# Optimization experiments

Hardware: AMD Instinct MI355X
Metric: run time of the kernel (lower is better)

## Reference

```python
import jax, jax.numpy as jnp
import numpy as np

B, T, D, H, CL = 2, 4096, 2048, 16, 512
DK = D // H          # key_dim == head_dim (value_factor=1) == 128
SCALING = DK ** -0.5


def _rel_pos():
    # RetNet relative position: per-head decay gamma, rotary sin/cos, chunk decay masks
    h = np.arange(H, dtype=np.float64)
    gamma = 1.0 - 2.0 ** (-5.0 - h)                           # (H,)
    angle = 1.0 / (10000.0 ** (np.arange(0, DK, 2) / DK))
    angle = np.repeat(angle, 2)                               # (DK,) each freq duplicated
    pos = np.arange(T)[:, None] * angle[None, :]              # (T, DK)
    sin, cos = np.sin(pos), np.cos(pos)
    idx = np.arange(CL)
    expn = idx[:, None] - idx[None, :]                        # (CL, CL)
    m = np.where(expn >= 0, gamma[:, None, None] ** np.maximum(expn, 0), 0.0)  # (H,CL,CL)
    scale = np.sqrt(m.sum(-1, keepdims=True))                 # (H,CL,1)
    mask = m / scale
    cross_decay = (gamma ** CL)[:, None, None]                # (H,1,1)
    inner = gamma[:, None] ** (idx + 1)                       # (H,CL)
    inner_decay = inner[:, :, None] / (scale / mask[:, -1].sum(-1)[:, None, None])  # (H,CL,1)
    f32 = lambda a: jnp.asarray(a, jnp.float32)
    return f32(sin), f32(cos), f32(mask), f32(cross_decay), f32(inner_decay)


def setup_inputs() -> dict:
    key = jax.random.key(0)
    kx, kq, kk, kv, kg, ko = jax.random.split(key, 6)
    sin, cos, mask, cross_decay, inner_decay = _rel_pos()
    mk = lambda k: jax.random.normal(k, (D, D), jnp.float32) * 0.02  # ~xavier w/ small gain
    z = jnp.zeros((D,), jnp.float32)
    return dict(
        x=jax.random.normal(kx, (B, T, D), jnp.float32),
        sin=sin, cos=cos, mask=mask, cross_decay=cross_decay, inner_decay=inner_decay,
        wq=mk(kq), bq=z, wk=mk(kk), bk=z, wv=mk(kv), bv=z, wg=mk(kg), bg=z,
        wo=jax.random.normal(ko, (D, D), jnp.float32) * (1.0 / np.sqrt(D)), bo=z,
    )


def _rotate_every_two(x):
    x1, x2 = x[..., ::2], x[..., 1::2]
    return jnp.stack((-x2, x1), axis=-1).reshape(x.shape)


def _theta_shift(x, sin, cos):
    return x * cos + _rotate_every_two(x) * sin


def reference(x, sin, cos, mask, cross_decay, inner_decay,
              wq, bq, wk, bk, wv, bv, wg, bg, wo, bo):
    NC = T // CL
    q = (x @ wq.T + bq).reshape(B, T, H, DK).transpose(0, 2, 1, 3)           # (B,H,T,DK)
    k = ((x @ wk.T + bk) * SCALING).reshape(B, T, H, DK).transpose(0, 2, 1, 3)
    v = x @ wv.T + bv                                                        # (B,T,D)
    g = x @ wg.T + bg
    qr = _theta_shift(q, sin, cos)
    kr = _theta_shift(k, sin, cos)
    # chunk views -> (B, NC, H, CL, DK)
    qr = qr.reshape(B, H, NC, CL, DK).transpose(0, 2, 1, 3, 4)
    kr = kr.reshape(B, H, NC, CL, DK).transpose(0, 2, 1, 3, 4)
    vc = v.reshape(B, NC, CL, H, DK).transpose(0, 1, 3, 2, 4)                # (B,NC,H,CL,HD)
    # intra-chunk decay-masked attention
    qk = jnp.einsum('bnhld,bnhmd->bnhlm', qr, kr) * mask                      # (B,NC,H,CL,CL)
    inner_scale = jnp.clip(jnp.abs(jax.lax.stop_gradient(qk)).sum(-1, keepdims=True), 1.0)
    inner_out = jnp.einsum('bnhlm,bnhmd->bnhld', qk / inner_scale, vc)
    # per-chunk KV contribution (keys weighted by remaining decay = last mask row)
    kv = jnp.einsum('bnhlk,bnhld->bnhkd', kr, vc * mask[:, -1, :, None])      # (B,NC,H,DK,HD)

    def step(carry, kv_i):
        kv_state, kv_scale = carry
        out = (kv_state / kv_scale, kv_scale)
        new_state = kv_state * cross_decay + kv_i
        s = jnp.abs(jax.lax.stop_gradient(new_state)).sum(-2, keepdims=True)
        new_scale = jnp.clip(s.max(-1, keepdims=True), 1.0)
        return (new_state, new_scale), out

    init = (jnp.zeros((B, H, DK, DK), x.dtype), jnp.ones((B, H, 1, 1), x.dtype))
    _, (kv_rec, cross_scale) = jax.lax.scan(step, init, jnp.moveaxis(kv, 1, 0))
    kv_rec = jnp.moveaxis(kv_rec, 0, 1)            # (B,NC,H,DK,HD)
    cross_scale = jnp.moveaxis(cross_scale, 0, 1)  # (B,NC,H,1,1)
    all_scale = jnp.maximum(inner_scale, cross_scale)
    cross_out = jnp.einsum('bnhlk,bnhkd->bnhld', qr * inner_decay, kv_rec)
    out = inner_out / (all_scale / inner_scale) + cross_out / (all_scale / cross_scale)
    out = out.transpose(0, 1, 3, 2, 4)             # (B,NC,CL,H,HD)
    # group_norm: LayerNorm over head_dim, no affine, eps=1e-6
    mu = out.mean(-1, keepdims=True)
    var = ((out - mu) ** 2).mean(-1, keepdims=True)
    out = (out - mu) / jnp.sqrt(var + 1e-6)
    out = out.reshape(B, T, D)
    out = jax.nn.silu(g) * out                     # swish gate
    return out @ wo.T + bo
```

## Files before the change

### kernel.cpp

```cpp
#include <hip/hip_runtime.h>
#include <hip/hip_bf16.h>
#include <math.h>

#define NB   2
#define NT   4096
#define ND   2048
#define NH   16
#define NDK  128
#define NCL  512
#define NNC  8
#define NTOK 8192
#define SCALING 0.08838834764831845f

typedef unsigned short u16;
typedef short short8 __attribute__((ext_vector_type(8)));
typedef unsigned short ushort8 __attribute__((ext_vector_type(8)));
typedef float f32x4 __attribute__((ext_vector_type(4)));
typedef float float4v __attribute__((ext_vector_type(4)));
typedef short short4v __attribute__((ext_vector_type(4)));

__device__ __forceinline__ float bf2f(u16 u) {
    union { unsigned int i; float f; } v; v.i = ((unsigned int)u) << 16; return v.f;
}
__device__ __forceinline__ u16 f2bf(float f) {
    union { float f; unsigned int i; } v; v.f = f;
    unsigned int r = v.i + 0x7FFFu + ((v.i >> 16) & 1u);
    return (u16)(r >> 16);
}

__device__ __forceinline__ void gload16(const void* g, void* l) {
    __builtin_amdgcn_global_load_lds(
        (const __attribute__((address_space(1))) unsigned int*)g,
        (__attribute__((address_space(3))) unsigned int*)l, 16, 0, 0);
}

#define MFMA16(acc_, a_, b_) acc_ = __builtin_amdgcn_mfma_f32_16x16x32_bf16(a_, b_, acc_, 0, 0, 0)

__device__ __forceinline__ void gemm_bt_core(
    const u16* __restrict__ A, const u16* __restrict__ Bm,
    int lda, int ldb, int K, u16* As, u16* Bs, f32x4 acc[4][4])
{
    const int tid  = threadIdx.x;
    const int lane = tid & 63;
    const int lr   = lane & 15;
    const int lg   = lane >> 4;
    const int wid  = tid >> 6;
    const int wr   = (wid >> 1) * 64;
    const int wc   = (wid & 1) * 64;
    const int swz  = lr & 7;
    const int uc0  = ((0 * 4 + lg) ^ swz) * 8;
    const int uc1  = ((1 * 4 + lg) ^ swz) * 8;

    for (int kt = 0; kt < K; kt += 64) {
#pragma unroll
        for (int i = 0; i < 4; ++i) {
            int c = tid + i * 256;
            int row = c >> 3, u = c & 7;
            int col = (u ^ (row & 7)) * 8;
            gload16(A  + (size_t)row * lda + kt + col, As + (size_t)c * 8);
            gload16(Bm + (size_t)row * ldb + kt + col, Bs + (size_t)c * 8);
        }
        __syncthreads();
#pragma unroll
        for (int kk = 0; kk < 2; ++kk) {
            const int uc = kk ? uc1 : uc0;
            short8 a[4], b[4];
#pragma unroll
            for (int m = 0; m < 4; ++m)
                a[m] = *(const short8*)(As + (size_t)(wr + m * 16 + lr) * 64 + uc);
#pragma unroll
            for (int n = 0; n < 4; ++n)
                b[n] = *(const short8*)(Bs + (size_t)(wc + n * 16 + lr) * 64 + uc);
#pragma unroll
            for (int m = 0; m < 4; ++m)
#pragma unroll
                for (int n = 0; n < 4; ++n)
                    MFMA16(acc[m][n], a[m], b[n]);
        }
        __syncthreads();
    }
}

__global__ __launch_bounds__(256) void k_f2bf(const float* __restrict__ src,
                                              u16* __restrict__ dst, int n4)
{
    int i = blockIdx.x * blockDim.x + threadIdx.x;
    int stride = gridDim.x * blockDim.x;
    for (int j = i; j < n4; j += stride) {
        float4v f = *(const float4v*)(src + (size_t)j * 4);
        short4v o;
        o.x = (short)f2bf(f.x); o.y = (short)f2bf(f.y);
        o.z = (short)f2bf(f.z); o.w = (short)f2bf(f.w);
        *(short4v*)(dst + (size_t)j * 4) = o;
    }
}

__global__ __launch_bounds__(256) void k_gemm1(
    const u16* __restrict__ xb, const u16* __restrict__ wb,
    const float* __restrict__ bq, const float* __restrict__ bk,
    const float* __restrict__ bv, const float* __restrict__ bg,
    const float* __restrict__ sinp, const float* __restrict__ cosp,
    const float* __restrict__ maskp,
    u16* __restrict__ qro, u16* __restrict__ kro, u16* __restrict__ krwT,
    u16* __restrict__ vT, u16* __restrict__ glin)
{
    __shared__ __align__(16) u16 As[128 * 64];
    __shared__ __align__(16) u16 Bs[128 * 64];
    f32x4 acc[4][4];
#pragma unroll
    for (int m = 0; m < 4; ++m)
#pragma unroll
        for (int n = 0; n < 4; ++n) acc[m][n] = (f32x4){0.f, 0.f, 0.f, 0.f};

    int bid = blockIdx.x;
    int swzb = (bid & 7) * 512 + (bid >> 3);
    int mt = swzb >> 6, nt = swzb & 63;

    gemm_bt_core(xb + (size_t)mt * 128 * ND, wb + (size_t)nt * 128 * ND,
                 ND, ND, ND, As, Bs, acc);

    int tid = threadIdx.x, lane = tid & 63, lr = lane & 15, lg = lane >> 4, wid = tid >> 6;
    int wr = (wid >> 1) * 64, wc = (wid & 1) * 64;
    int which = nt >> 4;

    if (which <= 1) {
        const float* bias = (which == 0) ? bq : bk;
#pragma unroll
        for (int m = 0; m < 4; ++m) {
#pragma unroll
            for (int n = 0; n < 4; ++n) {
#pragma unroll
                for (int r = 0; r < 4; ++r) {
                    int row = mt * 128 + wr + m * 16 + lg * 4 + r;
                    int col = nt * 128 + wc + n * 16 + lr;
                    int f = col & 2047, h = f >> 7, d = f & 127;
                    int b = row >> 12, t = row & 4095, cn = t >> 9, cl = t & 511;
                    float v = acc[m][n][r] + bias[f];
                    if (which == 1) v *= SCALING;
                    float sv = sinp[(size_t)t * NDK + d];
                    float cv = cosp[(size_t)t * NDK + d];
                    float vp = __shfl_xor(v, 1);
                    float rot = (lr & 1) ? vp : -vp;
                    float o = v * cv + rot * sv;
                    size_t chbase = (size_t)(b * NNC + cn) * NH + h;
                    if (which == 0) {
                        qro[(chbase * NCL + cl) * NDK + d] = f2bf(o);
                    } else {
                        kro[(chbase * NCL + cl) * NDK + d] = f2bf(o);
                        float w = maskp[((size_t)h * NCL + (NCL - 1)) * NCL + cl];
                        krwT[(chbase * NDK + d) * NCL + cl] = f2bf(o * w);
                    }
                }
            }
        }
    } else {
#pragma unroll
        for (int m = 0; m < 4; ++m) {
#pragma unroll
            for (int n = 0; n < 4; ++n) {
#pragma unroll
                for (int r = 0; r < 4; ++r) {
                    int row = mt * 128 + wr + m * 16 + lg * 4 + r;
                    int col = nt * 128 + wc + n * 16 + lr;
                    int f = col & 2047;
                    float v = acc[m][n][r];
                    if (which == 2) {
                        int h = f >> 7, d = f & 127;
                        int b = row >> 12, t = row & 4095, cn = t >> 9, cl = t & 511;
                        vT[(((size_t)(b * NNC + cn) * NH + h) * NDK + d) * NCL + cl] = f2bf(v + bv[f]);
                    } else {
                        glin[(size_t)row * ND + f] = f2bf(v + bg[f]);
                    }
                }
            }
        }
    }
}

__global__ __launch_bounds__(256) void k_gemm2(
    const u16* __restrict__ y, const u16* __restrict__ wob,
    const float* __restrict__ bo, float* __restrict__ out)
{
    __shared__ __align__(16) u16 As[128 * 64];
    __shared__ __align__(16) u16 Bs[128 * 64];
    f32x4 acc[4][4];
#pragma unroll
    for (int m = 0; m < 4; ++m)
#pragma unroll
        for (int n = 0; n < 4; ++n) acc[m][n] = (f32x4){0.f, 0.f, 0.f, 0.f};

    int bid = blockIdx.x;
    int swzb = (bid & 7) * 128 + (bid >> 3);
    int mt = swzb >> 4, nt = swzb & 15;

    gemm_bt_core(y + (size_t)mt * 128 * ND, wob + (size_t)nt * 128 * ND,
                 ND, ND, ND, As, Bs, acc);

    int tid = threadIdx.x, lane = tid & 63, lr = lane & 15, lg = lane >> 4, wid = tid >> 6;
    int wr = (wid >> 1) * 64, wc = (wid & 1) * 64;
#pragma unroll
    for (int m = 0; m < 4; ++m)
#pragma unroll
        for (int n = 0; n < 4; ++n)
#pragma unroll
            for (int r = 0; r < 4; ++r) {
                int row = mt * 128 + wr + m * 16 + lg * 4 + r;
                int col = nt * 128 + wc + n * 16 + lr;
                out[(size_t)row * ND + col] = acc[m][n][r] + bo[col];
            }
}

__global__ __launch_bounds__(256) void k_inner(
    const u16* __restrict__ qr, const u16* __restrict__ kr,
    const u16* __restrict__ vT, const float* __restrict__ mask,
    float* __restrict__ iraw, float* __restrict__ iscale)
{
    __shared__ __align__(16) u16 Qs[128 * 128];
    __shared__ __align__(16) u16 Ks[32 * 128];
    __shared__ __align__(16) u16 Vs[128 * 32];
    __shared__ __align__(16) u16 Ps[4][32 * 32];
    __shared__ float sl[128];

    int qt = blockIdx.x, bnh = blockIdx.y;
    int h = bnh & 15;
    const u16* Q = qr + (size_t)bnh * NCL * NDK + (size_t)qt * 128 * NDK;
    const u16* K = kr + (size_t)bnh * NCL * NDK;
    const u16* V = vT + (size_t)bnh * NDK * NCL;
    const float* M = mask + (size_t)h * NCL * NCL + (size_t)qt * 128 * NCL;

    int tid = threadIdx.x, lane = tid & 63, lr = lane & 15, lg = lane >> 4, wid = tid >> 6;
    if (tid < 128) sl[tid] = 0.f;
#pragma unroll
    for (int i = 0; i < 8; ++i) {
        int c = tid + i * 256;
        gload16(Q + (size_t)c * 8, (char*)Qs + (size_t)c * 16);
    }
    __syncthreads();

    short8 aq[2][4];
#pragma unroll
    for (int i = 0; i < 2; ++i)
#pragma unroll
        for (int kk = 0; kk < 4; ++kk)
            aq[i][kk] = *(const short8*)(Qs + (wid * 32 + i * 16 + lr) * 128 + kk * 32 + lg * 8);

    f32x4 acc[2][8];
#pragma unroll
    for (int i = 0; i < 2; ++i)
#pragma unroll
        for (int n = 0; n < 8; ++n) acc[i][n] = (f32x4){0.f, 0.f, 0.f, 0.f};

    int msteps = qt * 4 + 4;
    for (int ms = 0; ms < msteps; ++ms) {
        int mb = ms * 32;
#pragma unroll
        for (int i = 0; i < 2; ++i) {
            int c = tid + i * 256;
            int row = c >> 4, cc = (c & 15) * 8;
            gload16(K + (size_t)(mb + row) * NDK + cc, (char*)Ks + (size_t)c * 16);
        }
#pragma unroll
        for (int i = 0; i < 2; ++i) {
            int c = tid + i * 256;
            int row = c >> 2, cc = (c & 3) * 8;
            gload16(V + (size_t)row * NCL + mb + cc, (char*)Vs + (size_t)c * 16);
        }
        __syncthreads();

        f32x4 pa[2][2];
#pragma unroll
        for (int i = 0; i < 2; ++i) { pa[i][0] = (f32x4){0.f,0.f,0.f,0.f}; pa[i][1] = (f32x4){0.f,0.f,0.f,0.f}; }
#pragma unroll
        for (int kk = 0; kk < 4; ++kk) {
            short8 bk0 = *(const short8*)(Ks + (lr) * 128 + kk * 32 + lg * 8);
            short8 bk1 = *(const short8*)(Ks + (16 + lr) * 128 + kk * 32 + lg * 8);
#pragma unroll
            for (int i = 0; i < 2; ++i) {
                pa[i][0] = __builtin_amdgcn_mfma_f32_16x16x32_bf16(aq[i][kk], bk0, pa[i][0], 0, 0, 0);
                pa[i][1] = __builtin_amdgcn_mfma_f32_16x16x32_bf16(aq[i][kk], bk1, pa[i][1], 0, 0, 0);
            }
        }
#pragma unroll
        for (int i = 0; i < 2; ++i) {
#pragma unroll
            for (int r = 0; r < 4; ++r) {
                int rloc = i * 16 + lg * 4 + r;
                int row128 = wid * 32 + rloc;
                float m0 = M[(size_t)row128 * NCL + mb + lr];
                float m1 = M[(size_t)row128 * NCL + mb + 16 + lr];
                float p0 = pa[i][0][r] * m0;
                float p1 = pa[i][1][r] * m1;
                float ss = fabsf(p0) + fabsf(p1);
                ss += __shfl_xor(ss, 1); ss += __shfl_xor(ss, 2);
                ss += __shfl_xor(ss, 4); ss += __shfl_xor(ss, 8);
                if (lr == 0) sl[row128] += ss;
                Ps[wid][rloc * 32 + lr]      = f2bf(p0);
                Ps[wid][rloc * 32 + 16 + lr] = f2bf(p1);
            }
        }
        __syncthreads();

        short8 ap[2];
#pragma unroll
        for (int i = 0; i < 2; ++i)
            ap[i] = *(const short8*)(Ps[wid] + (i * 16 + lr) * 32 + lg * 8);
#pragma unroll
        for (int n = 0; n < 8; ++n) {
            short8 bv8 = *(const short8*)(Vs + (n * 16 + lr) * 32 + lg * 8);
#pragma unroll
            for (int i = 0; i < 2; ++i)
                acc[i][n] = __builtin_amdgcn_mfma_f32_16x16x32_bf16(ap[i], bv8, acc[i][n], 0, 0, 0);
        }
        __syncthreads();
    }

    float* OR = iraw + ((size_t)bnh * NCL + (size_t)qt * 128) * NDK;
#pragma unroll
    for (int i = 0; i < 2; ++i)
#pragma unroll
        for (int n = 0; n < 8; ++n)
#pragma unroll
            for (int r = 0; r < 4; ++r) {
                int row = wid * 32 + i * 16 + lg * 4 + r;
                int col = n * 16 + lr;
                OR[(size_t)row * NDK + col] = acc[i][n][r];
            }
    __syncthreads();
    if (tid < 128) iscale[(size_t)bnh * NCL + qt * 128 + tid] = fmaxf(1.f, sl[tid]);
}

__global__ __launch_bounds__(256) void k_kv(
    const u16* __restrict__ krwT, const u16* __restrict__ vT, float* __restrict__ kvi)
{
    __shared__ __align__(16) u16 As[128 * 64];
    __shared__ __align__(16) u16 Bs[128 * 64];
    f32x4 acc[4][4];
#pragma unroll
    for (int m = 0; m < 4; ++m)
#pragma unroll
        for (int n = 0; n < 4; ++n) acc[m][n] = (f32x4){0.f, 0.f, 0.f, 0.f};

    int bnh = blockIdx.x;
    gemm_bt_core(krwT + (size_t)bnh * NDK * NCL, vT + (size_t)bnh * NDK * NCL,
                 NCL, NCL, NCL, As, Bs, acc);

    int tid = threadIdx.x, lane = tid & 63, lr = lane & 15, lg = lane >> 4, wid = tid >> 6;
    int wr = (wid >> 1) * 64, wc = (wid & 1) * 64;
    float* O = kvi + (size_t)bnh * NDK * NDK;
#pragma unroll
    for (int m = 0; m < 4; ++m)
#pragma unroll
        for (int n = 0; n < 4; ++n)
#pragma unroll
            for (int r = 0; r < 4; ++r) {
                int row = wr + m * 16 + lg * 4 + r;
                int col = wc + n * 16 + lr;
                O[(size_t)row * NDK + col] = acc[m][n][r];
            }
}

__global__ __launch_bounds__(256) void k_scan(
    const float* __restrict__ kvi, const float* __restrict__ cdec,
    u16* __restrict__ kvrT, float* __restrict__ csc)
{
    int bh = blockIdx.x;
    int b = bh >> 4, h = bh & 15;
    float cd = cdec[h];
    int tid = threadIdx.x;
    int col = tid & 127;
    int r0 = (tid >> 7) * 64;
    float st[64];
#pragma unroll
    for (int i = 0; i < 64; ++i) st[i] = 0.f;
    float scale = 1.f;
    __shared__ float cs[128];
    __shared__ float scsh;

    for (int n = 0; n < NNC; ++n) {
        size_t idx = (size_t)((b * NNC + n) * NH + h);
        size_t kb = idx * (NDK * NDK);
        float inv = 1.f / scale;
#pragma unroll
        for (int i = 0; i < 64; ++i)
            kvrT[kb + (size_t)col * NDK + r0 + i] = f2bf(st[i] * inv);
        if (tid == 0) csc[idx] = scale;

        const float* KV = kvi + kb;
        float colsum = 0.f;
#pragma unroll
        for (int i = 0; i < 64; ++i) {
            float xv = st[i] * cd + KV[(size_t)(r0 + i) * NDK + col];
            st[i] = xv;
            colsum += fabsf(xv);
        }
        __syncthreads();
        if (tid < 128) cs[tid] = 0.f;
        __syncthreads();
        atomicAdd(&cs[col], colsum);
        __syncthreads();
        if (tid == 0) {
            float mx = cs[0];
            for (int i = 1; i < 128; ++i) mx = fmaxf(mx, cs[i]);
            scsh = fmaxf(1.f, mx);
        }
        __syncthreads();
        scale = scsh;
    }
}

__global__ __launch_bounds__(256) void k_combine(
    const u16* __restrict__ qr, const u16* __restrict__ kvrT,
    const float* __restrict__ iraw, const float* __restrict__ iscale,
    const float* __restrict__ cscale, const float* __restrict__ idecay,
    const u16* __restrict__ glin, u16* __restrict__ y)
{
    __shared__ __align__(16) u16 As[128 * 64];
    __shared__ __align__(16) u16 Bs[128 * 64];
    __shared__ float ssum[128];
    __shared__ float ssq[128];
    f32x4 acc[4][4];
#pragma unroll
    for (int m = 0; m < 4; ++m)
#pragma unroll
        for (int n = 0; n < 4; ++n) acc[m][n] = (f32x4){0.f, 0.f, 0.f, 0.f};

    int qt = blockIdx.x, bnh = blockIdx.y;
    int b = bnh >> 7, cn = (bnh >> 4) & 7, h = bnh & 15;
    gemm_bt_core(qr + (size_t)bnh * NCL * NDK + (size_t)qt * 128 * NDK,
                 kvrT + (size_t)bnh * NDK * NDK, NDK, NDK, NDK, As, Bs, acc);

    int tid = threadIdx.x, lane = tid & 63, lr = lane & 15, lg = lane >> 4, wid = tid >> 6;
    int wr = (wid >> 1) * 64, wc = (wid & 1) * 64;
    if (tid < 128) { ssum[tid] = 0.f; ssq[tid] = 0.f; }
    __syncthreads();
    float csv = cscale[bnh];

#pragma unroll
    for (int m = 0; m < 4; ++m) {
#pragma unroll
        for (int r = 0; r < 4; ++r) {
            int rloc = wr + m * 16 + lg * 4 + r;
            int l = qt * 128 + rloc;
            float isc = iscale[(size_t)bnh * NCL + l];
            float all = fmaxf(isc, csv);
            float c1 = 1.f / all;
            float c2 = (csv / all) * idecay[h * NCL + l];
            const float* ir = iraw + ((size_t)bnh * NCL + l) * NDK;
            float lsum = 0.f, lsq = 0.f;
#pragma unroll
            for (int n = 0; n < 4; ++n) {
                int col = wc + n * 16 + lr;
                float v = ir[col] * c1 + acc[m][n][r] * c2;
                acc[m][n][r] = v;
                lsum += v; lsq += v * v;
            }
            lsum += __shfl_xor(lsum, 1); lsum += __shfl_xor(lsum, 2);
            lsum += __shfl_xor(lsum, 4); lsum += __shfl_xor(lsum, 8);
            lsq  += __shfl_xor(lsq, 1);  lsq  += __shfl_xor(lsq, 2);
            lsq  += __shfl_xor(lsq, 4);  lsq  += __shfl_xor(lsq, 8);
            if (lr == 0) { atomicAdd(&ssum[rloc], lsum); atomicAdd(&ssq[rloc], lsq); }
        }
    }
    __syncthreads();
#pragma unroll
    for (int m = 0; m < 4; ++m) {
#pragma unroll
        for (int r = 0; r < 4; ++r) {
            int rloc = wr + m * 16 + lg * 4 + r;
            int l = qt * 128 + rloc;
            float mu = ssum[rloc] * (1.f / 128.f);
            float var = ssq[rloc] * (1.f / 128.f) - mu * mu;
            float rstd = rsqrtf(fmaxf(var, 0.f) + 1e-6f);
            int t = cn * NCL + l;
            size_t obase = ((size_t)(b * NT + t)) * ND + (size_t)h * NDK;
#pragma unroll
            for (int n = 0; n < 4; ++n) {
                int col = wc + n * 16 + lr;
                float gv = bf2f(glin[obase + col]);
                float sg = gv / (1.f + expf(-gv));
                float ov = (acc[m][n][r] - mu) * rstd * sg;
                y[obase + col] = f2bf(ov);
            }
        }
    }
}

extern "C" void kernel_launch(void* const* d_in, const int* in_sizes, int n_in,
                              void* d_out, int out_size, void* d_ws, size_t ws_size,
                              hipStream_t stream)
{
    const float* x    = (const float*)d_in[0];
    const float* sinp = (const float*)d_in[1];
    const float* cosp = (const float*)d_in[2];
    const float* mask = (const float*)d_in[3];
    const float* cdec = (const float*)d_in[4];
    const float* idec = (const float*)d_in[5];
    const float* wq   = (const float*)d_in[6];
    const float* bq   = (const float*)d_in[7];
    const float* wk   = (const float*)d_in[8];
    const float* bk   = (const float*)d_in[9];
    const float* wv   = (const float*)d_in[10];
    const float* bv   = (const float*)d_in[11];
    const float* wg   = (const float*)d_in[12];
    const float* bg   = (const float*)d_in[13];
    const float* wo   = (const float*)d_in[14];
    const float* bo   = (const float*)d_in[15];
    float* out = (float*)d_out;

    char* ws = (char*)d_ws;
    u16*   XB   = (u16*)(ws + 0);
    u16*   WB   = (u16*)(ws + 33554432);
    u16*   WOB  = (u16*)(ws + 67108864);
    u16*   QR   = (u16*)(ws + 75497472);
    u16*   KR   = (u16*)(ws + 109051904);
    u16*   KRWT = (u16*)(ws + 142606336);
    u16*   VT   = (u16*)(ws + 176160768);
    u16*   GLIN = (u16*)(ws + 209715200);
    float* KVI  = (float*)(ws + 243269632);
    float* CSC  = (float*)(ws + 260046848);
    float* IRAW = (float*)(ws + 0);
    u16*   Y    = KR;
    u16*   KVRT = KRWT;
    float* ISC  = (float*)(ws + 243269632);

    k_f2bf<<<2048, 256, 0, stream>>>(x, XB, 4194304);
    k_f2bf<<<1024, 256, 0, stream>>>(wq, WB,            1048576);
    k_f2bf<<<1024, 256, 0, stream>>>(wk, WB + 4194304,  1048576);
    k_f2bf<<<1024, 256, 0, stream>>>(wv, WB + 8388608,  1048576);
    k_f2bf<<<1024, 256, 0, stream>>>(wg, WB + 12582912, 1048576);
    k_f2bf<<<1024, 256, 0, stream>>>(wo, WOB,           1048576);

    k_gemm1<<<4096, 256, 0, stream>>>(XB, WB, bq, bk, bv, bg, sinp, cosp, mask,
                                      QR, KR, KRWT, VT, GLIN);
    k_kv<<<256, 256, 0, stream>>>(KRWT, VT, KVI);
    k_scan<<<32, 256, 0, stream>>>(KVI, cdec, KVRT, CSC);
    k_inner<<<dim3(4, 256), 256, 0, stream>>>(QR, KR, VT, mask, IRAW, ISC);
    k_combine<<<dim3(4, 256), 256, 0, stream>>>(QR, KVRT, IRAW, ISC, CSC, idec, GLIN, Y);
    k_gemm2<<<1024, 256, 0, stream>>>(Y, WOB, bo, out);
}
```

Before: 975.6 us.

## Triple-buffer GEMM core with BK=32 async LDS prefetch and raw barriers

```diff
diff --git a/kernel.cpp b/kernel.cpp
--- a/kernel.cpp
+++ b/kernel.cpp
@@ -35,50 +35,87 @@
 }
 
 #define MFMA16(acc_, a_, b_) acc_ = __builtin_amdgcn_mfma_f32_16x16x32_bf16(a_, b_, acc_, 0, 0, 0)
-
-__device__ __forceinline__ void gemm_bt_core(
-    const u16* __restrict__ A, const u16* __restrict__ Bm,
-    int lda, int ldb, int K, u16* As, u16* Bs, f32x4 acc[4][4])
-{
+#define SBAR  asm volatile("s_barrier" ::: "memory")
+
+
+__device__ __forceinline__ void stage32(const u16* __restrict__ g, int ld,
+                                        u16* lds, int tid)
+{
+#pragma unroll
+    for (int j = 0; j < 2; ++j) {
+        int c = tid + j * 256;
+        int row = c >> 2, u = c & 3;
+        int col = (u ^ ((row >> 1) & 3)) * 8;
+        gload16(g + (size_t)row * ld + col, lds + (size_t)c * 8);
+    }
+}
+
+__device__ __forceinline__ void tile_step(
+    int t, int nt,
+    const u16* __restrict__ Aop, const u16* __restrict__ Bop,
+    int lda, int ldb, int tid, int arow, int brow, int uc,
+    u16* ARd, u16* BRd, u16* AW, u16* BW, f32x4 acc[4][4])
+{
+    if (t + 2 < nt) {
+        stage32(Aop + (size_t)(t + 2) * 32, lda, AW, tid);
+        stage32(Bop + (size_t)(t + 2) * 32, ldb, BW, tid);
+    }
+    short8 a[4], b[4];
+#pragma unroll
+    for (int m = 0; m < 4; ++m)
+        a[m] = *(const short8*)(ARd + (size_t)(arow + m * 16) * 32 + uc);
+#pragma unroll
+    for (int n = 0; n < 4; ++n)
+        b[n] = *(const short8*)(BRd + (size_t)(brow + n * 16) * 32 + uc);
+    __builtin_amdgcn_s_setprio(1);
+#pragma unroll
+    for (int m = 0; m < 4; ++m)
+#pragma unroll
+        for (int n = 0; n < 4; ++n)
+            MFMA16(acc[m][n], a[m], b[n]);
+    __builtin_amdgcn_s_setprio(0);
+    if (t + 2 < nt)
+        asm volatile("s_waitcnt vmcnt(4)" ::: "memory");
+    else
+        asm volatile("s_waitcnt vmcnt(0)" ::: "memory");
+    SBAR;
+}
+
+template<int KDIM>
+__device__ __forceinline__ void gemm_bt3(
+    const u16* __restrict__ Aop, const u16* __restrict__ Bop,
+    int lda, int ldb,
+    u16* A0, u16* A1, u16* A2, u16* B0, u16* B1, u16* B2,
+    f32x4 acc[4][4])
+{
+    constexpr int NTt = KDIM / 32;
     const int tid  = threadIdx.x;
     const int lane = tid & 63;
     const int lr   = lane & 15;
     const int lg   = lane >> 4;
     const int wid  = tid >> 6;
-    const int wr   = (wid >> 1) * 64;
-    const int wc   = (wid & 1) * 64;
-    const int swz  = lr & 7;
-    const int uc0  = ((0 * 4 + lg) ^ swz) * 8;
-    const int uc1  = ((1 * 4 + lg) ^ swz) * 8;
-
-    for (int kt = 0; kt < K; kt += 64) {
-#pragma unroll
-        for (int i = 0; i < 4; ++i) {
-            int c = tid + i * 256;
-            int row = c >> 3, u = c & 7;
-            int col = (u ^ (row & 7)) * 8;
-            gload16(A  + (size_t)row * lda + kt + col, As + (size_t)c * 8);
-            gload16(Bm + (size_t)row * ldb + kt + col, Bs + (size_t)c * 8);
-        }
-        __syncthreads();
-#pragma unroll
-        for (int kk = 0; kk < 2; ++kk) {
-            const int uc = kk ? uc1 : uc0;
-            short8 a[4], b[4];
-#pragma unroll
-            for (int m = 0; m < 4; ++m)
-                a[m] = *(const short8*)(As + (size_t)(wr + m * 16 + lr) * 64 + uc);
-#pragma unroll
-            for (int n = 0; n < 4; ++n)
-                b[n] = *(const short8*)(Bs + (size_t)(wc + n * 16 + lr) * 64 + uc);
-#pragma unroll
-            for (int m = 0; m < 4; ++m)
-#pragma unroll
-                for (int n = 0; n < 4; ++n)
-                    MFMA16(acc[m][n], a[m], b[n]);
-        }
-        __syncthreads();
-    }
+    const int arow = (wid >> 1) * 64 + lr;
+    const int brow = (wid & 1) * 64 + lr;
+    const int uc   = (lg ^ ((lr >> 1) & 3)) * 8;
+
+    stage32(Aop,      lda, A0, tid);
+    stage32(Bop,      ldb, B0, tid);
+    stage32(Aop + 32, lda, A1, tid);
+    stage32(Bop + 32, ldb, B1, tid);
+    asm volatile("s_waitcnt vmcnt(4)" ::: "memory");
+    SBAR;
+
+    int t = 0;
+    while (t + 3 <= NTt) {
+        tile_step(t,     NTt, Aop, Bop, lda, ldb, tid, arow, brow, uc, A0, B0, A2, B2, acc);
+        tile_step(t + 1, NTt, Aop, Bop, lda, ldb, tid, arow, brow, uc, A1, B1, A0, B0, acc);
+        tile_step(t + 2, NTt, Aop, Bop, lda, ldb, tid, arow, brow, uc, A2, B2, A1, B1, acc);
+        t += 3;
+    }
+    if (t < NTt)
+        tile_step(t, NTt, Aop, Bop, lda, ldb, tid, arow, brow, uc, A0, B0, A2, B2, acc);
+    if (t + 1 < NTt)
+        tile_step(t + 1, NTt, Aop, Bop, lda, ldb, tid, arow, brow, uc, A1, B1, A0, B0, acc);
 }
 
 __global__ __launch_bounds__(256) void k_f2bf(const float* __restrict__ src,
@@ -95,7 +132,7 @@
     }
 }
 
-__global__ __launch_bounds__(256) void k_gemm1(
+__global__ __launch_bounds__(256, 3) void k_gemm1(
     const u16* __restrict__ xb, const u16* __restrict__ wb,
     const float* __restrict__ bq, const float* __restrict__ bk,
     const float* __restrict__ bv, const float* __restrict__ bg,
@@ -104,8 +141,12 @@
     u16* __restrict__ qro, u16* __restrict__ kro, u16* __restrict__ krwT,
     u16* __restrict__ vT, u16* __restrict__ glin)
 {
-    __shared__ __align__(16) u16 As[128 * 64];
-    __shared__ __align__(16) u16 Bs[128 * 64];
+    __shared__ __align__(16) u16 A0[128 * 32];
+    __shared__ __align__(16) u16 A1[128 * 32];
+    __shared__ __align__(16) u16 A2[128 * 32];
+    __shared__ __align__(16) u16 B0[128 * 32];
+    __shared__ __align__(16) u16 B1[128 * 32];
+    __shared__ __align__(16) u16 B2[128 * 32];
     f32x4 acc[4][4];
 #pragma unroll
     for (int m = 0; m < 4; ++m)
@@ -114,10 +155,10 @@
 
     int bid = blockIdx.x;
     int swzb = (bid & 7) * 512 + (bid >> 3);
-    int mt = swzb >> 6, nt = swzb & 63;
-
-    gemm_bt_core(xb + (size_t)mt * 128 * ND, wb + (size_t)nt * 128 * ND,
-                 ND, ND, ND, As, Bs, acc);
+    int nt = swzb >> 6, mt = swzb & 63;
+
+    gemm_bt3<ND>(xb + (size_t)mt * 128 * ND, wb + (size_t)nt * 128 * ND,
+                 ND, ND, A0, A1, A2, B0, B1, B2, acc);
 
     int tid = threadIdx.x, lane = tid & 63, lr = lane & 15, lg = lane >> 4, wid = tid >> 6;
     int wr = (wid >> 1) * 64, wc = (wid & 1) * 64;
@@ -177,12 +218,16 @@
     }
 }
 
-__global__ __launch_bounds__(256) void k_gemm2(
+__global__ __launch_bounds__(256, 3) void k_gemm2(
     const u16* __restrict__ y, const u16* __restrict__ wob,
     const float* __restrict__ bo, float* __restrict__ out)
 {
-    __shared__ __align__(16) u16 As[128 * 64];
-    __shared__ __align__(16) u16 Bs[128 * 64];
+    __shared__ __align__(16) u16 A0[128 * 32];
+    __shared__ __align__(16) u16 A1[128 * 32];
+    __shared__ __align__(16) u16 A2[128 * 32];
+    __shared__ __align__(16) u16 B0[128 * 32];
+    __shared__ __align__(16) u16 B1[128 * 32];
+    __shared__ __align__(16) u16 B2[128 * 32];
     f32x4 acc[4][4];
 #pragma unroll
     for (int m = 0; m < 4; ++m)
@@ -191,10 +236,10 @@
 
     int bid = blockIdx.x;
     int swzb = (bid & 7) * 128 + (bid >> 3);
-    int mt = swzb >> 4, nt = swzb & 15;
-
-    gemm_bt_core(y + (size_t)mt * 128 * ND, wob + (size_t)nt * 128 * ND,
-                 ND, ND, ND, As, Bs, acc);
+    int nt = swzb >> 6, mt = swzb & 63;
+
+    gemm_bt3<ND>(y + (size_t)mt * 128 * ND, wob + (size_t)nt * 128 * ND,
+                 ND, ND, A0, A1, A2, B0, B1, B2, acc);
 
     int tid = threadIdx.x, lane = tid & 63, lr = lane & 15, lg = lane >> 4, wid = tid >> 6;
     int wr = (wid >> 1) * 64, wc = (wid & 1) * 64;
@@ -329,11 +374,15 @@
     if (tid < 128) iscale[(size_t)bnh * NCL + qt * 128 + tid] = fmaxf(1.f, sl[tid]);
 }
 
-__global__ __launch_bounds__(256) void k_kv(
+__global__ __launch_bounds__(256, 3) void k_kv(
     const u16* __restrict__ krwT, const u16* __restrict__ vT, float* __restrict__ kvi)
 {
-    __shared__ __align__(16) u16 As[128 * 64];
-    __shared__ __align__(16) u16 Bs[128 * 64];
+    __shared__ __align__(16) u16 A0[128 * 32];
+    __shared__ __align__(16) u16 A1[128 * 32];
+    __shared__ __align__(16) u16 A2[128 * 32];
+    __shared__ __align__(16) u16 B0[128 * 32];
+    __shared__ __align__(16) u16 B1[128 * 32];
+    __shared__ __align__(16) u16 B2[128 * 32];
     f32x4 acc[4][4];
 #pragma unroll
     for (int m = 0; m < 4; ++m)
@@ -341,8 +390,8 @@
         for (int n = 0; n < 4; ++n) acc[m][n] = (f32x4){0.f, 0.f, 0.f, 0.f};
 
     int bnh = blockIdx.x;
-    gemm_bt_core(krwT + (size_t)bnh * NDK * NCL, vT + (size_t)bnh * NDK * NCL,
-                 NCL, NCL, NCL, As, Bs, acc);
+    gemm_bt3<NCL>(krwT + (size_t)bnh * NDK * NCL, vT + (size_t)bnh * NDK * NCL,
+                  NCL, NCL, A0, A1, A2, B0, B1, B2, acc);
 
     int tid = threadIdx.x, lane = tid & 63, lr = lane & 15, lg = lane >> 4, wid = tid >> 6;
     int wr = (wid >> 1) * 64, wc = (wid & 1) * 64;
@@ -408,14 +457,18 @@
     }
 }
 
-__global__ __launch_bounds__(256) void k_combine(
+__global__ __launch_bounds__(256, 3) void k_combine(
     const u16* __restrict__ qr, const u16* __restrict__ kvrT,
     const float* __restrict__ iraw, const float* __restrict__ iscale,
     const float* __restrict__ cscale, const float* __restrict__ idecay,
     const u16* __restrict__ glin, u16* __restrict__ y)
 {
-    __shared__ __align__(16) u16 As[128 * 64];
-    __shared__ __align__(16) u16 Bs[128 * 64];
+    __shared__ __align__(16) u16 A0[128 * 32];
+    __shared__ __align__(16) u16 A1[128 * 32];
+    __shared__ __align__(16) u16 A2[128 * 32];
+    __shared__ __align__(16) u16 B0[128 * 32];
+    __shared__ __align__(16) u16 B1[128 * 32];
+    __shared__ __align__(16) u16 B2[128 * 32];
     __shared__ float ssum[128];
     __shared__ float ssq[128];
     f32x4 acc[4][4];
@@ -426,8 +479,9 @@
 
     int qt = blockIdx.x, bnh = blockIdx.y;
     int b = bnh >> 7, cn = (bnh >> 4) & 7, h = bnh & 15;
-    gemm_bt_core(qr + (size_t)bnh * NCL * NDK + (size_t)qt * 128 * NDK,
-                 kvrT + (size_t)bnh * NDK * NDK, NDK, NDK, NDK, As, Bs, acc);
+    gemm_bt3<NDK>(qr + (size_t)bnh * NCL * NDK + (size_t)qt * 128 * NDK,
+                  kvrT + (size_t)bnh * NDK * NDK, NDK, NDK,
+                  A0, A1, A2, B0, B1, B2, acc);
 
     int tid = threadIdx.x, lane = tid & 63, lr = lane & 15, lg = lane >> 4, wid = tid >> 6;
     int wr = (wid >> 1) * 64, wc = (wid & 1) * 64;
```

Result: slower. 1.033 ms (+5.9%).
